# Optimization experiments

Hardware: AMD Instinct MI355X
Metric: run time of the kernel (lower is better)

The kernel has to match this reference:

```python
import jax, jax.numpy as jnp
import numpy as np

B, C_IN, H, W = 8, 64, 64, 64
C_OUT = 128
K, STRIDE, PAD = 3, 1, 1
GRID_MIN, GRID_MAX, NUM_GRIDS = -2.0, 2.0, 8
FEAT = C_IN * K * K  # 576


def setup_inputs() -> dict:
    key = jax.random.key(0)
    k1, k2, k3 = jax.random.split(key, 3)
    x = jax.random.normal(k1, (B, C_IN, H, W), dtype=jnp.float32)
    grid = jnp.linspace(GRID_MIN, GRID_MAX, NUM_GRIDS, dtype=jnp.float32)
    spline_weight = jax.random.normal(k2, (FEAT * NUM_GRIDS, C_OUT), dtype=jnp.float32) * 0.1
    # nn.Linear default init ~ U(-1/sqrt(in), 1/sqrt(in)); stored as (in, out) for x @ W
    bound = 1.0 / np.sqrt(FEAT)
    kw, kb = jax.random.split(k3)
    base_w = jax.random.uniform(kw, (FEAT, C_OUT), dtype=jnp.float32, minval=-bound, maxval=bound)
    base_b = jax.random.uniform(kb, (C_OUT,), dtype=jnp.float32, minval=-bound, maxval=bound)
    return {"x": x, "grid": grid, "spline_weight": spline_weight,
            "base_w": base_w, "base_b": base_b}


def reference(x, grid, spline_weight, base_w, base_b):
    b, c, h, w = x.shape
    # F.unfold equivalent: patches in (channel, kh, kw) channel-major order.
    patches = jax.lax.conv_general_dilated_patches(
        x, filter_shape=(K, K), window_strides=(STRIDE, STRIDE),
        padding=((PAD, PAD), (PAD, PAD)))  # [B, C*K*K, H', W']
    oh, ow = patches.shape[2], patches.shape[3]
    # -> [B*L, FEAT] rows, matching unfold().transpose(1,2).reshape(...)
    p = patches.reshape(b, FEAT, oh * ow).transpose(0, 2, 1).reshape(-1, FEAT)
    # RBF basis expansion: exp(-((x - g) / h)^2), h = grid spacing
    denom = (GRID_MAX - GRID_MIN) / (NUM_GRIDS - 1)
    basis = jnp.exp(-(((p[:, :, None] - grid) / denom) ** 2))  # [N, FEAT, G]
    ret = basis.reshape(p.shape[0], FEAT * NUM_GRIDS) @ spline_weight  # [N, C_OUT]
    ret = ret + jax.nn.silu(p) @ base_w + base_b
    # [B, L, C_OUT] -> [B, C_OUT, H', W']
    out = ret.reshape(b, oh * ow, C_OUT).transpose(0, 2, 1).reshape(b, C_OUT, oh, ow)
    return out
```

## Files before the change

### kernel.cpp

```cpp
#include <hip/hip_runtime.h>

#define C_IN   64
#define HW_DIM 64
#define C_OUT  128
#define NG     8
#define KSPL   4608
#define BM     64
#define BK     64
#define NSPL_STEPS 72
#define NSTEPS 81
#define NPAD   66
#define NEXP   (8 * C_IN * NPAD * NPAD)

#define WT_BYTES 1327104
#define XE_OFF   WT_BYTES
#define XE_BYTES (NEXP * NG * 2)
#define SE_OFF   (XE_OFF + XE_BYTES)

typedef __attribute__((ext_vector_type(8))) __bf16 bf16x8;
typedef __attribute__((ext_vector_type(4))) float  f32x4;

__global__ __launch_bounds__(256)
void prep_wt(const float* __restrict__ sw, const float* __restrict__ bw,
             __bf16* __restrict__ wt3)
{
  const int step = blockIdx.x;
  const int t    = threadIdx.x;
  const int wc   = t >> 6;
  const int lane = t & 63;
  const int l15  = lane & 15;
  const int g4   = lane >> 4;
#pragma unroll
  for (int n = 0; n < 2; ++n)
#pragma unroll
    for (int ks = 0; ks < 2; ++ks) {
      const int co = wc * 32 + n * 16 + l15;
      bf16x8 v;
#pragma unroll
      for (int e = 0; e < 8; ++e) {
        const int k = step * 64 + ks * 32 + g4 * 8 + e;
        float f;
        if (k < KSPL) f = sw[(size_t)k * C_OUT + co];
        else          f = bw[(size_t)(k - KSPL) * C_OUT + co];
        v[e] = (__bf16)f;
      }
      *(bf16x8*)(wt3 + (size_t)step * 8192 + wc * 2048 + (n * 2 + ks) * 512
                 + lane * 8) = v;
    }
}

__global__ __launch_bounds__(256)
void expand(const float* __restrict__ x, const float* __restrict__ grid,
            __bf16* __restrict__ xe, __bf16* __restrict__ se)
{
  const int idx = blockIdx.x * 256 + threadIdx.x;
  if (idx >= NEXP) return;
  const int xp = idx % NPAD;
  const int r  = idx / NPAD;
  const int yp = r % NPAD;
  const int bc = r / NPAD;

  float p = 0.f;
  if (xp >= 1 && xp <= HW_DIM && yp >= 1 && yp <= HW_DIM)
    p = x[(size_t)bc * (HW_DIM * HW_DIM) + (yp - 1) * HW_DIM + (xp - 1)];

  bf16x8 v;
#pragma unroll
  for (int g = 0; g < NG; ++g) {
    const float z = 1.75f * (p - grid[g]);
    v[g] = (__bf16)__expf(-z * z);
  }
  *(bf16x8*)(xe + (size_t)idx * NG) = v;
  const float e = __expf(-p);
  se[idx] = (__bf16)(p * __builtin_amdgcn_rcpf(1.f + e));
}

__global__ __launch_bounds__(256, 2)
void kan_gemm(const __bf16* __restrict__ xe, const __bf16* __restrict__ se,
              const __bf16* __restrict__ wt3, const float* __restrict__ base_b,
              float* __restrict__ out)
{
  __shared__ __align__(16) __bf16 As[2][BM][BK];
  __shared__ int tbl[576];

  const int t    = threadIdx.x;
  const int lane = t & 63;
  const int wid  = t >> 6;
  const int l15  = lane & 15;
  const int g4   = lane >> 4;

  const int bid = blockIdx.x;
  const int swz = (bid & 7) * 64 + (bid >> 3);
  const int b   = swz >> 6;
  const int y0  = swz & 63;

  for (int f = t; f < 576; f += 256) {
    const int c  = f / 9;
    const int j  = f - 9 * c;
    const int kh = j / 3;
    const int kw = j - 3 * kh;
    tbl[f] = c * 4356 + kh * 66 + kw;
  }

  const int F0  = b * 278784 + y0 * 66 + l15;
  const int F0s = b * 278784 + y0 * 66 + (t & 63);

  f32x4 acc[2][4];
#pragma unroll
  for (int n = 0; n < 2; ++n)
#pragma unroll
    for (int m = 0; m < 4; ++m)
      acc[n][m] = f32x4{0.f, 0.f, 0.f, 0.f};

  auto loadB = [&](bf16x8 wf[2][2], int step) {
    const __bf16* wb = wt3 + (size_t)step * 8192 + wid * 2048 + lane * 8;
#pragma unroll
    for (int n = 0; n < 2; ++n)
#pragma unroll
      for (int ks = 0; ks < 2; ++ks)
        wf[n][ks] = *(const bf16x8*)(wb + (n * 2 + ks) * 512);
  };

  auto loadA = [&](bf16x8 xf[4][2], int step) {
#pragma unroll
    for (int ks = 0; ks < 2; ++ks) {
      const int f = step * 8 + ks * 4 + g4;
      const __bf16* ab = xe + ((size_t)(F0 + tbl[f])) * 8;
#pragma unroll
      for (int m = 0; m < 4; ++m)
        xf[m][ks] = *(const bf16x8*)(ab + m * 128);
    }
  };

  auto mfmaS = [&](bf16x8 xf[4][2], bf16x8 wf[2][2]) {
#pragma unroll
    for (int ks = 0; ks < 2; ++ks)
#pragma unroll
      for (int n = 0; n < 2; ++n)
#pragma unroll
        for (int m = 0; m < 4; ++m)
          acc[n][m] = __builtin_amdgcn_mfma_f32_16x16x32_bf16(
              wf[n][ks], xf[m][ks], acc[n][m], 0, 0, 0);
  };

  __syncthreads();

  bf16x8 xfA[4][2], xfB[4][2], wfA[2][2], wfB[2][2];
  loadA(xfA, 0); loadB(wfA, 0);
  for (int s = 0; s < NSPL_STEPS - 2; s += 2) {
    loadA(xfB, s + 1); loadB(wfB, s + 1);
    mfmaS(xfA, wfA);
    loadA(xfA, s + 2); loadB(wfA, s + 2);
    mfmaS(xfB, wfB);
  }
  loadA(xfB, NSPL_STEPS - 1); loadB(wfB, NSPL_STEPS - 1);
  mfmaS(xfA, wfA);
  mfmaS(xfB, wfB);

  auto stageA = [&](int buf, int bs) {
    const int q  = t >> 6;
    const int px = t & 63;
#pragma unroll
    for (int h = 0; h < 2; ++h) {
      const int gran = q + h * 4;
      bf16x8 v;
#pragma unroll
      for (int jj = 0; jj < 8; ++jj) {
        const int f = (bs - NSPL_STEPS) * 64 + gran * 8 + jj;
        v[jj] = se[(size_t)(F0s + tbl[f])];
      }
      *(bf16x8*)(&As[buf][px][(gran ^ (px & 7)) * 8]) = v;
    }
  };

  stageA(0, NSPL_STEPS);
  __syncthreads();
  for (int bs = NSPL_STEPS; bs < NSTEPS; ++bs) {
    const int cb = (bs - NSPL_STEPS) & 1;
    if (bs + 1 < NSTEPS) stageA(cb ^ 1, bs + 1);
    loadB(wfA, bs);
    bf16x8 xf[4][2];
#pragma unroll
    for (int ks = 0; ks < 2; ++ks)
#pragma unroll
      for (int m = 0; m < 4; ++m) {
        const int pr = m * 16 + l15;
        xf[m][ks] = *(const bf16x8*)(&As[cb][pr][(((ks * 4 + g4) ^ (pr & 7)) * 8)]);
      }
    mfmaS(xf, wfA);
    __syncthreads();
  }

#pragma unroll
  for (int n = 0; n < 2; ++n) {
    const int co = wid * 32 + n * 16 + g4 * 4;
#pragma unroll
    for (int m = 0; m < 4; ++m) {
      const int pl = m * 16 + l15;
      float* o = out + (size_t)(b * C_OUT + co) * 4096 + y0 * 64 + pl;
#pragma unroll
      for (int i = 0; i < 4; ++i)
        o[(size_t)i * 4096] = acc[n][m][i] + base_b[co + i];
    }
  }
}

extern "C" void kernel_launch(void* const* d_in, const int* in_sizes, int n_in,
                              void* d_out, int out_size, void* d_ws, size_t ws_size,
                              hipStream_t stream) {
  const float* x    = (const float*)d_in[0];
  const float* grid = (const float*)d_in[1];
  const float* sw   = (const float*)d_in[2];
  const float* bw   = (const float*)d_in[3];
  const float* bb   = (const float*)d_in[4];
  float* out = (float*)d_out;

  __bf16* wt3 = (__bf16*)d_ws;
  __bf16* xe  = (__bf16*)((char*)d_ws + XE_OFF);
  __bf16* se  = (__bf16*)((char*)d_ws + SE_OFF);

  prep_wt<<<NSTEPS, 256, 0, stream>>>(sw, bw, wt3);
  expand<<<(NEXP + 255) / 256, 256, 0, stream>>>(x, grid, xe, se);
  kan_gemm<<<512, 256, 0, stream>>>(xe, se, wt3, bb, out);
}
```

Baseline: 92.97 us.

## Split GEMM block into eight waves of sixteen output channels each

The GEMM kernel goes from 4 waves per block, each computing 32 output channels, to 8 waves per block, each computing 16. The weight layout is repacked to match, and the shared-memory staging for the base-branch tile is spread over the 512 threads. The aim is more waves in flight to hide gather and load latency. The cost is that every wave still loads the full A fragment, so A-fragment traffic per MFMA doubles. The tighter launch bounds may also cap registers per wave and force spills.

```diff
diff --git a/kernel.cpp b/kernel.cpp
--- a/kernel.cpp
+++ b/kernel.cpp
@@ -6,7 +6,6 @@
 #define NG     8
 #define KSPL   4608
 #define BM     64
-#define BK     64
 #define NSPL_STEPS 72
 #define NSTEPS 81
 #define NPAD   66
@@ -22,19 +21,19 @@
 
 __global__ __launch_bounds__(256)
 void prep_wt(const float* __restrict__ sw, const float* __restrict__ bw,
-             __bf16* __restrict__ wt3)
+             __bf16* __restrict__ wt4)
 {
   const int step = blockIdx.x;
   const int t    = threadIdx.x;
-  const int wc   = t >> 6;
   const int lane = t & 63;
   const int l15  = lane & 15;
   const int g4   = lane >> 4;
 #pragma unroll
-  for (int n = 0; n < 2; ++n)
+  for (int i = 0; i < 2; ++i) {
+    const int wid = (t >> 6) + i * 4;
+    const int co  = wid * 16 + l15;
 #pragma unroll
     for (int ks = 0; ks < 2; ++ks) {
-      const int co = wc * 32 + n * 16 + l15;
       bf16x8 v;
 #pragma unroll
       for (int e = 0; e < 8; ++e) {
@@ -44,9 +43,9 @@
         else          f = bw[(size_t)(k - KSPL) * C_OUT + co];
         v[e] = (__bf16)f;
       }
-      *(bf16x8*)(wt3 + (size_t)step * 8192 + wc * 2048 + (n * 2 + ks) * 512
-                 + lane * 8) = v;
+      *(bf16x8*)(wt4 + (size_t)step * 8192 + wid * 1024 + ks * 512 + lane * 8) = v;
     }
+  }
 }
 
 __global__ __launch_bounds__(256)
@@ -75,12 +74,12 @@
   se[idx] = (__bf16)(p * __builtin_amdgcn_rcpf(1.f + e));
 }
 
-__global__ __launch_bounds__(256, 2)
+__global__ __launch_bounds__(512, 4)
 void kan_gemm(const __bf16* __restrict__ xe, const __bf16* __restrict__ se,
-              const __bf16* __restrict__ wt3, const float* __restrict__ base_b,
+              const __bf16* __restrict__ wt4, const float* __restrict__ base_b,
               float* __restrict__ out)
 {
-  __shared__ __align__(16) __bf16 As[2][BM][BK];
+  __shared__ __align__(16) __bf16 As[2][BM][64];
   __shared__ int tbl[576];
 
   const int t    = threadIdx.x;
@@ -94,7 +93,7 @@
   const int b   = swz >> 6;
   const int y0  = swz & 63;
 
-  for (int f = t; f < 576; f += 256) {
+  for (int f = t; f < 576; f += 512) {
     const int c  = f / 9;
     const int j  = f - 9 * c;
     const int kh = j / 3;
@@ -105,20 +104,15 @@
   const int F0  = b * 278784 + y0 * 66 + l15;
   const int F0s = b * 278784 + y0 * 66 + (t & 63);
 
-  f32x4 acc[2][4];
-#pragma unroll
-  for (int n = 0; n < 2; ++n)
-#pragma unroll
-    for (int m = 0; m < 4; ++m)
-      acc[n][m] = f32x4{0.f, 0.f, 0.f, 0.f};
-
-  auto loadB = [&](bf16x8 wf[2][2], int step) {
-    const __bf16* wb = wt3 + (size_t)step * 8192 + wid * 2048 + lane * 8;
-#pragma unroll
-    for (int n = 0; n < 2; ++n)
-#pragma unroll
-      for (int ks = 0; ks < 2; ++ks)
-        wf[n][ks] = *(const bf16x8*)(wb + (n * 2 + ks) * 512);
+  f32x4 acc[4];
+#pragma unroll
+  for (int m = 0; m < 4; ++m) acc[m] = f32x4{0.f, 0.f, 0.f, 0.f};
+
+  auto loadB = [&](bf16x8 wf[2], int step) {
+    const __bf16* wb = wt4 + (size_t)step * 8192 + wid * 1024 + lane * 8;
+#pragma unroll
+    for (int ks = 0; ks < 2; ++ks)
+      wf[ks] = *(const bf16x8*)(wb + ks * 512);
   };
 
   auto loadA = [&](bf16x8 xf[4][2], int step) {
@@ -132,20 +126,18 @@
     }
   };
 
-  auto mfmaS = [&](bf16x8 xf[4][2], bf16x8 wf[2][2]) {
+  auto mfmaS = [&](bf16x8 xf[4][2], bf16x8 wf[2]) {
 #pragma unroll
     for (int ks = 0; ks < 2; ++ks)
 #pragma unroll
-      for (int n = 0; n < 2; ++n)
-#pragma unroll
-        for (int m = 0; m < 4; ++m)
-          acc[n][m] = __builtin_amdgcn_mfma_f32_16x16x32_bf16(
-              wf[n][ks], xf[m][ks], acc[n][m], 0, 0, 0);
+      for (int m = 0; m < 4; ++m)
+        acc[m] = __builtin_amdgcn_mfma_f32_16x16x32_bf16(
+            wf[ks], xf[m][ks], acc[m], 0, 0, 0);
   };
 
   __syncthreads();
 
-  bf16x8 xfA[4][2], xfB[4][2], wfA[2][2], wfB[2][2];
+  bf16x8 xfA[4][2], xfB[4][2], wfA[2], wfB[2];
   loadA(xfA, 0); loadB(wfA, 0);
   for (int s = 0; s < NSPL_STEPS - 2; s += 2) {
     loadA(xfB, s + 1); loadB(wfB, s + 1);
@@ -160,17 +152,13 @@
   auto stageA = [&](int buf, int bs) {
     const int q  = t >> 6;
     const int px = t & 63;
-#pragma unroll
-    for (int h = 0; h < 2; ++h) {
-      const int gran = q + h * 4;
-      bf16x8 v;
-#pragma unroll
-      for (int jj = 0; jj < 8; ++jj) {
-        const int f = (bs - NSPL_STEPS) * 64 + gran * 8 + jj;
-        v[jj] = se[(size_t)(F0s + tbl[f])];
-      }
-      *(bf16x8*)(&As[buf][px][(gran ^ (px & 7)) * 8]) = v;
+    bf16x8 v;
+#pragma unroll
+    for (int jj = 0; jj < 8; ++jj) {
+      const int f = (bs - NSPL_STEPS) * 64 + q * 8 + jj;
+      v[jj] = se[(size_t)(F0s + tbl[f])];
     }
+    *(bf16x8*)(&As[buf][px][(q ^ (px & 7)) * 8]) = v;
   };
 
   stageA(0, NSPL_STEPS);
@@ -191,17 +179,14 @@
     __syncthreads();
   }
 
-#pragma unroll
-  for (int n = 0; n < 2; ++n) {
-    const int co = wid * 32 + n * 16 + g4 * 4;
-#pragma unroll
-    for (int m = 0; m < 4; ++m) {
-      const int pl = m * 16 + l15;
-      float* o = out + (size_t)(b * C_OUT + co) * 4096 + y0 * 64 + pl;
-#pragma unroll
-      for (int i = 0; i < 4; ++i)
-        o[(size_t)i * 4096] = acc[n][m][i] + base_b[co + i];
-    }
+  const int co = wid * 16 + g4 * 4;
+#pragma unroll
+  for (int m = 0; m < 4; ++m) {
+    const int pl = m * 16 + l15;
+    float* o = out + (size_t)(b * C_OUT + co) * 4096 + y0 * 64 + pl;
+#pragma unroll
+    for (int i = 0; i < 4; ++i)
+      o[(size_t)i * 4096] = acc[m][i] + base_b[co + i];
   }
 }
 
@@ -215,11 +200,11 @@
   const float* bb   = (const float*)d_in[4];
   float* out = (float*)d_out;
 
-  __bf16* wt3 = (__bf16*)d_ws;
+  __bf16* wt4 = (__bf16*)d_ws;
   __bf16* xe  = (__bf16*)((char*)d_ws + XE_OFF);
   __bf16* se  = (__bf16*)((char*)d_ws + SE_OFF);
 
-  prep_wt<<<NSTEPS, 256, 0, stream>>>(sw, bw, wt3);
+  prep_wt<<<NSTEPS, 256, 0, stream>>>(sw, bw, wt4);
   expand<<<(NEXP + 255) / 256, 256, 0, stream>>>(x, grid, xe, se);
-  kan_gemm<<<512, 256, 0, stream>>>(xe, se, wt3, bb, out);
-}
+  kan_gemm<<<512, 512, 0, stream>>>(xe, se, wt4, bb, out);
+}
```

Measured after the change: 118.2 us. +27.1%, slower.

## Stage spline A-tiles into LDS via global_load_lds instead of per-warp register loads

Applied to the files above, without the earlier changes.

The spline phase loaded expanded activations from global memory straight into registers, and each of the four waves fetched the same 64x64 A-tile on its own. Now the block copies each A-tile once into a double-buffered, XOR-swizzled LDS buffer using direct global-to-LDS loads. MFMA operands are then read from LDS. This cuts redundant global and L2 traffic four-fold, at the cost of two block barriers per step and LDS read overhead.

```diff
diff --git a/kernel.cpp b/kernel.cpp
--- a/kernel.cpp
+++ b/kernel.cpp
@@ -6,7 +6,6 @@
 #define NG     8
 #define KSPL   4608
 #define BM     64
-#define BK     64
 #define NSPL_STEPS 72
 #define NSTEPS 81
 #define NPAD   66
@@ -75,12 +74,18 @@
   se[idx] = (__bf16)(p * __builtin_amdgcn_rcpf(1.f + e));
 }
 
+static __device__ __forceinline__ void gload16(const __bf16* g, __bf16* l) {
+  __builtin_amdgcn_global_load_lds(
+      (const __attribute__((address_space(1))) void*)g,
+      (__attribute__((address_space(3))) void*)l, 16, 0, 0);
+}
+
 __global__ __launch_bounds__(256, 2)
 void kan_gemm(const __bf16* __restrict__ xe, const __bf16* __restrict__ se,
               const __bf16* __restrict__ wt3, const float* __restrict__ base_b,
               float* __restrict__ out)
 {
-  __shared__ __align__(16) __bf16 As[2][BM][BK];
+  __shared__ __align__(16) __bf16 As[2][BM][64];
   __shared__ int tbl[576];
 
   const int t    = threadIdx.x;
@@ -102,8 +107,10 @@
     tbl[f] = c * 4356 + kh * 66 + kw;
   }
 
-  const int F0  = b * 278784 + y0 * 66 + l15;
-  const int F0s = b * 278784 + y0 * 66 + (t & 63);
+  const int ROW = b * 278784 + y0 * 66;
+
+  const int qsrc = (lane & 7) ^ ((lane >> 3) & 7);
+  const int pbase = (wid << 3) + (lane >> 3);
 
   f32x4 acc[2][4];
 #pragma unroll
@@ -112,6 +119,13 @@
     for (int m = 0; m < 4; ++m)
       acc[n][m] = f32x4{0.f, 0.f, 0.f, 0.f};
 
+  auto stageA = [&](int buf, int step) {
+    const int off = ROW + tbl[step * 8 + qsrc] + pbase;
+    __bf16* dst = &As[buf][0][0] + t * 8;
+    gload16(xe + (size_t)off * 8,        dst);
+    gload16(xe + (size_t)(off + 32) * 8, dst + 2048);
+  };
+
   auto loadB = [&](bf16x8 wf[2][2], int step) {
     const __bf16* wb = wt3 + (size_t)step * 8192 + wid * 2048 + lane * 8;
 #pragma unroll
@@ -121,18 +135,15 @@
         wf[n][ks] = *(const bf16x8*)(wb + (n * 2 + ks) * 512);
   };
 
-  auto loadA = [&](bf16x8 xf[4][2], int step) {
-#pragma unroll
-    for (int ks = 0; ks < 2; ++ks) {
-      const int f = step * 8 + ks * 4 + g4;
-      const __bf16* ab = xe + ((size_t)(F0 + tbl[f])) * 8;
-#pragma unroll
-      for (int m = 0; m < 4; ++m)
-        xf[m][ks] = *(const bf16x8*)(ab + m * 128);
-    }
-  };
-
-  auto mfmaS = [&](bf16x8 xf[4][2], bf16x8 wf[2][2]) {
+  auto compute = [&](int buf, bf16x8 wf[2][2]) {
+    bf16x8 xf[4][2];
+#pragma unroll
+    for (int ks = 0; ks < 2; ++ks)
+#pragma unroll
+      for (int m = 0; m < 4; ++m) {
+        const int pr = m * 16 + l15;
+        xf[m][ks] = *(const bf16x8*)(&As[buf][pr][(((ks * 4 + g4) ^ (pr & 7)) * 8)]);
+      }
 #pragma unroll
     for (int ks = 0; ks < 2; ++ks)
 #pragma unroll
@@ -145,49 +156,41 @@
 
   __syncthreads();
 
-  bf16x8 xfA[4][2], xfB[4][2], wfA[2][2], wfB[2][2];
-  loadA(xfA, 0); loadB(wfA, 0);
-  for (int s = 0; s < NSPL_STEPS - 2; s += 2) {
-    loadA(xfB, s + 1); loadB(wfB, s + 1);
-    mfmaS(xfA, wfA);
-    loadA(xfA, s + 2); loadB(wfA, s + 2);
-    mfmaS(xfB, wfB);
-  }
-  loadA(xfB, NSPL_STEPS - 1); loadB(wfB, NSPL_STEPS - 1);
-  mfmaS(xfA, wfA);
-  mfmaS(xfB, wfB);
-
-  auto stageA = [&](int buf, int bs) {
-    const int q  = t >> 6;
+  bf16x8 wfA[2][2], wfB[2][2];
+  stageA(0, 0); loadB(wfA, 0);
+  __syncthreads();
+  for (int s = 0; s < NSPL_STEPS; s += 2) {
+    if (s + 1 < NSPL_STEPS) { stageA(1, s + 1); loadB(wfB, s + 1); }
+    compute(0, wfA);
+    __syncthreads();
+    if (s + 2 < NSPL_STEPS) { stageA(0, s + 2); loadB(wfA, s + 2); }
+    compute(1, wfB);
+    __syncthreads();
+  }
+
+  const int ROWs = ROW + (t & 63);
+  auto stageBase = [&](int buf, int bs) {
     const int px = t & 63;
 #pragma unroll
     for (int h = 0; h < 2; ++h) {
-      const int gran = q + h * 4;
+      const int q = (t >> 6) + h * 4;
       bf16x8 v;
 #pragma unroll
       for (int jj = 0; jj < 8; ++jj) {
-        const int f = (bs - NSPL_STEPS) * 64 + gran * 8 + jj;
-        v[jj] = se[(size_t)(F0s + tbl[f])];
+        const int f = (bs - NSPL_STEPS) * 64 + q * 8 + jj;
+        v[jj] = se[(size_t)(ROWs + tbl[f])];
       }
-      *(bf16x8*)(&As[buf][px][(gran ^ (px & 7)) * 8]) = v;
+      *(bf16x8*)(&As[buf][px][(q ^ (px & 7)) * 8]) = v;
     }
   };
 
-  stageA(0, NSPL_STEPS);
+  stageBase(0, NSPL_STEPS);
   __syncthreads();
   for (int bs = NSPL_STEPS; bs < NSTEPS; ++bs) {
     const int cb = (bs - NSPL_STEPS) & 1;
-    if (bs + 1 < NSTEPS) stageA(cb ^ 1, bs + 1);
+    if (bs + 1 < NSTEPS) stageBase(cb ^ 1, bs + 1);
     loadB(wfA, bs);
-    bf16x8 xf[4][2];
-#pragma unroll
-    for (int ks = 0; ks < 2; ++ks)
-#pragma unroll
-      for (int m = 0; m < 4; ++m) {
-        const int pr = m * 16 + l15;
-        xf[m][ks] = *(const bf16x8*)(&As[cb][pr][(((ks * 4 + g4) ^ (pr & 7)) * 8)]);
-      }
-    mfmaS(xf, wfA);
+    compute(cb, wfA);
     __syncthreads();
   }
 
```

Result: faster. 87.36 us (-6.0%).
